# Kernel tuning notes

Hardware: AMD Instinct MI355X
Metric: run time of the kernel (lower is better)

Reference implementation:

```python
import jax, jax.numpy as jnp
import numpy as np

B, C, H, W = 4, 256, 64, 64
DQK = C // 8  # 32
EPS = 1e-5

def conv1x1(x, Wt, b):
    # 1x1 conv == per-pixel channel matmul. x: [B,C,H,W], Wt: [O,C], b: [O]
    return jnp.einsum('bchw,oc->bohw', x, Wt) + b[None, :, None, None]

def setup_inputs() -> dict:
    key = jax.random.key(0)
    ks = jax.random.split(key, 4)
    s = 1.0 / np.sqrt(C)
    return {
        'x': jax.random.normal(ks[0], (B, C, H, W), dtype=jnp.float32),
        'Wq': jax.random.normal(ks[1], (DQK, C), dtype=jnp.float32) * s,
        'bq': jnp.zeros((DQK,), dtype=jnp.float32),
        'Wk': jax.random.normal(ks[2], (DQK, C), dtype=jnp.float32) * s,
        'bk': jnp.zeros((DQK,), dtype=jnp.float32),
        'Wv': jax.random.normal(ks[3], (C, C), dtype=jnp.float32) * s,
        'bv': jnp.zeros((C,), dtype=jnp.float32),
        'bn_gamma': jnp.ones((C,), dtype=jnp.float32),
        'bn_beta': jnp.zeros((C,), dtype=jnp.float32),
    }

def reference(x, Wq, bq, Wk, bk, Wv, bv, bn_gamma, bn_beta):
    b, c, h, w = x.shape
    n = h * w
    q = conv1x1(x, Wq, bq).reshape(b, -1, n)   # [B, C/8, N]
    k = conv1x1(x, Wk, bk).reshape(b, -1, n)   # [B, C/8, N]
    v = conv1x1(x, Wv, bv).reshape(b, -1, n)   # [B, C,   N]
    # attention_weights = softmax(Q^T K) over last dim (no 1/sqrt(d) scaling)
    attn = jax.nn.softmax(jnp.einsum('bdi,bdj->bij', q, k), axis=-1)  # [B,N,N]
    out = jnp.einsum('bci,bij->bcj', v, attn).reshape(b, c, h, w)
    # BatchNorm2d (training mode: batch stats over B,H,W, biased var)
    mean = jnp.mean(out, axis=(0, 2, 3), keepdims=True)
    var = jnp.var(out, axis=(0, 2, 3), keepdims=True)
    out = (out - mean) * jax.lax.rsqrt(var + EPS)
    out = out * bn_gamma[None, :, None, None] + bn_beta[None, :, None, None]
    return x + out * 1e-05
```

## Files before the change

### kernel.cpp

```cpp
#include <hip/hip_runtime.h>
#include <hip/hip_bf16.h>

#define NB 4
#define NC 256
#define NN 4096

typedef __bf16 bf16x8 __attribute__((ext_vector_type(8)));
typedef float f32x4 __attribute__((ext_vector_type(4)));
typedef float f32x16 __attribute__((ext_vector_type(16)));
typedef unsigned short u16x4 __attribute__((ext_vector_type(4)));
typedef unsigned short u16x8 __attribute__((ext_vector_type(8)));
typedef unsigned int u32x2 __attribute__((ext_vector_type(2)));
typedef unsigned int u32x4 __attribute__((ext_vector_type(4)));

#if __has_builtin(__builtin_amdgcn_exp2f)
#define EXP2(x) __builtin_amdgcn_exp2f(x)
#else
#define EXP2(x) exp2f(x)
#endif

#define LOG2E 1.4426950408889634f

__device__ __forceinline__ unsigned short f2bf(float f) {
  union { __bf16 h; unsigned short u; } v;
  v.h = (__bf16)f;
  return v.u;
}
__device__ __forceinline__ float bf2f(unsigned short h) {
  union { unsigned u; float f; } v; v.u = ((unsigned)h) << 16;
  return v.f;
}

__device__ __forceinline__ u32x2 lane32swap(unsigned a, unsigned b) {
#if __has_builtin(__builtin_amdgcn_permlane32_swap)
  return __builtin_amdgcn_permlane32_swap(a, b, false, false);
#else
  unsigned ca = __shfl_xor(a, 32), cb = __shfl_xor(b, 32);
  int h = (threadIdx.x & 63) >> 5;
  u32x2 r; r[0] = h ? cb : a; r[1] = h ? b : ca;
  return r;
#endif
}

__global__ __launch_bounds__(256) void k0_prep(const float* __restrict__ Wq,
                                               const float* __restrict__ Wk,
                                               const float* __restrict__ Wv,
                                               unsigned short* __restrict__ Wcat,
                                               unsigned short* __restrict__ Wvb,
                                               float* __restrict__ stats) {
  int tid = blockIdx.x * 256 + threadIdx.x;
  int nt = gridDim.x * 256;
  for (int i = tid; i < 64 * NC; i += nt) {
    int d = i >> 8, c = i & 255;
    float v = (d < 32) ? Wq[d * NC + c] : Wk[(d - 32) * NC + c];
    Wcat[i] = f2bf(v);
  }
  for (int i = tid; i < NC * NC; i += nt) Wvb[i] = f2bf(Wv[i]);
  for (int i = tid; i < 1024; i += nt) stats[i] = 0.f;
}

__global__ __launch_bounds__(256) void k1_cvt_tr(const float* __restrict__ x,
                                                 unsigned short* __restrict__ xbf,
                                                 unsigned short* __restrict__ xT) {
  __shared__ __align__(16) unsigned short lt[64][68];
  int bid = blockIdx.x;
  int b  = bid >> 8;
  int cb = (bid >> 6) & 3;
  int nb = bid & 63;
  int c0 = cb * 64, n0 = nb * 64;
  int t = threadIdx.x;
  int tc = t >> 4;
  int tn = (t & 15) * 4;
#pragma unroll
  for (int it = 0; it < 4; ++it) {
    int c = c0 + tc + it * 16;
    f32x4 xv = *reinterpret_cast<const f32x4*>(&x[((size_t)b * NC + c) * NN + n0 + tn]);
    u16x4 hv;
    hv[0] = f2bf(xv[0]); hv[1] = f2bf(xv[1]); hv[2] = f2bf(xv[2]); hv[3] = f2bf(xv[3]);
    *reinterpret_cast<u16x4*>(&xbf[((size_t)b * NC + c) * NN + n0 + tn]) = hv;
    *reinterpret_cast<u16x4*>(&lt[tc + it * 16][tn]) = hv;
  }
  __syncthreads();
  int nl = t >> 2;
  int cl0 = (t & 3) * 16;
  u16x8 o0, o1;
#pragma unroll
  for (int q = 0; q < 8; ++q) o0[q] = lt[cl0 + q][nl];
#pragma unroll
  for (int q = 0; q < 8; ++q) o1[q] = lt[cl0 + 8 + q][nl];
  size_t ro = ((size_t)b * NN + n0 + nl) * NC + c0 + cl0;
  *reinterpret_cast<u16x8*>(&xT[ro]) = o0;
  *reinterpret_cast<u16x8*>(&xT[ro + 8]) = o1;
}

__global__ __launch_bounds__(256, 2) void k2_qk(const unsigned short* __restrict__ xT,
                                                const unsigned short* __restrict__ Wcat,
                                                const float* __restrict__ bq,
                                                const float* __restrict__ bk,
                                                unsigned short* __restrict__ Qt,
                                                unsigned short* __restrict__ Kt) {
  __shared__ __align__(16) unsigned short lt2[64][72];
  int bid = blockIdx.x;
  int b = bid >> 6, it = bid & 63;
  int i0 = it * 64;
  int t = threadIdx.x;
  int w = t >> 6, l = t & 63, l15 = l & 15, g = l >> 4;

  f32x4 acc[4];
#pragma unroll
  for (int f = 0; f < 4; ++f) acc[f] = f32x4{0.f, 0.f, 0.f, 0.f};

  const unsigned short* xrow = &xT[((size_t)b * NN + i0 + w * 16 + l15) * NC];
#pragma unroll
  for (int ks = 0; ks < 8; ++ks) {
    bf16x8 a = *reinterpret_cast<const bf16x8*>(&xrow[ks * 32 + g * 8]);
#pragma unroll
    for (int f = 0; f < 4; ++f) {
      bf16x8 bb = *reinterpret_cast<const bf16x8*>(&Wcat[(f * 16 + l15) * NC + ks * 32 + g * 8]);
      acc[f] = __builtin_amdgcn_mfma_f32_16x16x32_bf16(a, bb, acc[f], 0, 0, 0);
    }
  }
#pragma unroll
  for (int f = 0; f < 4; ++f) {
    int d = f * 16 + l15;
    float bias = (f < 2) ? bq[d] : bk[d - 32];
    float scale = (f < 2) ? LOG2E : 1.0f;
#pragma unroll
    for (int r = 0; r < 4; ++r)
      lt2[w * 16 + g * 4 + r][d] = f2bf((acc[f][r] + bias) * scale);
  }
  __syncthreads();
  int il = t >> 2, quad = t & 3;
  u32x4 v0 = *reinterpret_cast<const u32x4*>(&lt2[il][quad * 16]);
  u32x4 v1 = *reinterpret_cast<const u32x4*>(&lt2[il][quad * 16 + 8]);
  unsigned short* dst = (quad < 2) ? &Qt[((size_t)b * NN + i0 + il) * 32 + quad * 16]
                                   : &Kt[((size_t)b * NN + i0 + il) * 32 + (quad - 2) * 16];
  *reinterpret_cast<u32x4*>(dst) = v0;
  *reinterpret_cast<u32x4*>(&dst[8]) = v1;
}

__global__ __launch_bounds__(256, 4) void k3_rowsum(const unsigned short* __restrict__ Qt,
                                                    const unsigned short* __restrict__ Kt,
                                                    float* __restrict__ Lrow) {
  __shared__ float sred[4][16];
  int bid = blockIdx.x;
  int b = bid >> 8, it = bid & 255;
  int i0 = it * 16;
  int t = threadIdx.x, w = t >> 6, l = t & 63, l15 = l & 15, g = l >> 4;
  bf16x8 a = *reinterpret_cast<const bf16x8*>(&Qt[((size_t)b * NN + i0 + l15) * 32 + g * 8]);
  float rs0 = 0.f, rs1 = 0.f, rs2 = 0.f, rs3 = 0.f;
  int jbase = w * 1024;
  for (int jc = 0; jc < 16; ++jc) {
    int jb = jbase + jc * 64;
#pragma unroll
    for (int f = 0; f < 4; ++f) {
      bf16x8 bb = *reinterpret_cast<const bf16x8*>(&Kt[((size_t)b * NN + jb + f * 16 + l15) * 32 + g * 8]);
      f32x4 s = __builtin_amdgcn_mfma_f32_16x16x32_bf16(a, bb, f32x4{0.f, 0.f, 0.f, 0.f}, 0, 0, 0);
      rs0 += EXP2(s[0]); rs1 += EXP2(s[1]); rs2 += EXP2(s[2]); rs3 += EXP2(s[3]);
    }
  }
#pragma unroll
  for (int m = 1; m < 16; m <<= 1) {
    rs0 += __shfl_xor(rs0, m); rs1 += __shfl_xor(rs1, m);
    rs2 += __shfl_xor(rs2, m); rs3 += __shfl_xor(rs3, m);
  }
  if (l15 == 0) {
    sred[w][g * 4 + 0] = rs0; sred[w][g * 4 + 1] = rs1;
    sred[w][g * 4 + 2] = rs2; sred[w][g * 4 + 3] = rs3;
  }
  __syncthreads();
  if (t < 16) {
    float d = sred[0][t] + sred[1][t] + sred[2][t] + sred[3][t];
    Lrow[(size_t)b * NN + i0 + t] = -__log2f(d);
  }
}

__global__ __launch_bounds__(256, 2) void k4_attn(const unsigned short* __restrict__ xbf,
                                                  const unsigned short* __restrict__ Qt,
                                                  const unsigned short* __restrict__ Kt,
                                                  const float* __restrict__ Lrow,
                                                  unsigned short* __restrict__ Tt,
                                                  float* __restrict__ scol) {
  __shared__ __align__(16) unsigned short xlds[2][16384];
  int bid = blockIdx.x;
  int ih = bid & 1;
  int b  = (bid >> 1) & 3;
  int jt = bid >> 3;
  int t = threadIdx.x, w = t >> 6;
  int jw = w >> 1, cw = w & 1;
  int l = t & 63, l31 = l & 31, h = l >> 5;
  int j0 = jt * 64 + jw * 32;
  int c0 = cw * 128;
  const size_t qbase = (size_t)b * NN;
  unsigned short* Tt_p = Tt + (size_t)ih * ((size_t)NB * NN * NC);
  float* scol_p = scol + (size_t)ih * (NB * NN);
  int i0base = ih * 2048;
  int crow = t >> 3;
  int slot = t & 7;

  bf16x8 bk0 = *reinterpret_cast<const bf16x8*>(&Kt[(qbase + j0 + l31) * 32 + h * 8]);
  bf16x8 bk1 = *reinterpret_cast<const bf16x8*>(&Kt[(qbase + j0 + l31) * 32 + 16 + h * 8]);

  f32x16 acc0 = {0}, acc1 = {0}, acc2 = {0}, acc3 = {0};
  float cs = 0.f;
  u32x4 sreg0, sreg1, sreg2, sreg3, sreg4, sreg5, sreg6, sreg7;

#define REGLOAD(ibase_)                                                              \
  {                                                                                  \
    const unsigned short* xb_ = &xbf[(size_t)b * NC * NN + (ibase_) + slot * 8];     \
    sreg0 = *reinterpret_cast<const u32x4*>(&xb_[(size_t)(0 * 32 + crow) * NN]);     \
    sreg1 = *reinterpret_cast<const u32x4*>(&xb_[(size_t)(1 * 32 + crow) * NN]);     \
    sreg2 = *reinterpret_cast<const u32x4*>(&xb_[(size_t)(2 * 32 + crow) * NN]);     \
    sreg3 = *reinterpret_cast<const u32x4*>(&xb_[(size_t)(3 * 32 + crow) * NN]);     \
    sreg4 = *reinterpret_cast<const u32x4*>(&xb_[(size_t)(4 * 32 + crow) * NN]);     \
    sreg5 = *reinterpret_cast<const u32x4*>(&xb_[(size_t)(5 * 32 + crow) * NN]);     \
    sreg6 = *reinterpret_cast<const u32x4*>(&xb_[(size_t)(6 * 32 + crow) * NN]);     \
    sreg7 = *reinterpret_cast<const u32x4*>(&xb_[(size_t)(7 * 32 + crow) * NN]);     \
  }

#define DSWRITE(buf_)                                                                \
  {                                                                                  \
    int gsw_ = (slot ^ (crow & 7)) * 8;                                              \
    unsigned short* lb_ = &xlds[buf_][crow * 64 + gsw_];                             \
    *reinterpret_cast<u32x4*>(&lb_[0 * 2048]) = sreg0;                               \
    *reinterpret_cast<u32x4*>(&lb_[1 * 2048]) = sreg1;                               \
    *reinterpret_cast<u32x4*>(&lb_[2 * 2048]) = sreg2;                               \
    *reinterpret_cast<u32x4*>(&lb_[3 * 2048]) = sreg3;                               \
    *reinterpret_cast<u32x4*>(&lb_[4 * 2048]) = sreg4;                               \
    *reinterpret_cast<u32x4*>(&lb_[5 * 2048]) = sreg5;                               \
    *reinterpret_cast<u32x4*>(&lb_[6 * 2048]) = sreg6;                               \
    *reinterpret_cast<u32x4*>(&lb_[7 * 2048]) = sreg7;                               \
  }

  REGLOAD(i0base);
  DSWRITE(0);
  __syncthreads();
  int buf = 0;

  for (int st = 0; st < 32; ++st) {
    int ibase = i0base + st * 64;
    if (st + 1 < 32) REGLOAD(ibase + 64);
    const unsigned short* xt = xlds[buf];
#pragma unroll
    for (int ks = 0; ks < 2; ++ks) {
      int isub = ibase + ks * 32;
      const float* Lb = &Lrow[qbase + isub + 4 * h];
      f32x4 l0 = *reinterpret_cast<const f32x4*>(&Lb[0]);
      f32x4 l1 = *reinterpret_cast<const f32x4*>(&Lb[8]);
      f32x4 l2 = *reinterpret_cast<const f32x4*>(&Lb[16]);
      f32x4 l3 = *reinterpret_cast<const f32x4*>(&Lb[24]);
      f32x16 s;
#pragma unroll
      for (int r = 0; r < 4; ++r) { s[r] = l0[r]; s[4 + r] = l1[r]; s[8 + r] = l2[r]; s[12 + r] = l3[r]; }
      bf16x8 aq0 = *reinterpret_cast<const bf16x8*>(&Qt[(qbase + isub + l31) * 32 + h * 8]);
      bf16x8 aq1 = *reinterpret_cast<const bf16x8*>(&Qt[(qbase + isub + l31) * 32 + 16 + h * 8]);
      s = __builtin_amdgcn_mfma_f32_32x32x16_bf16(aq0, bk0, s, 0, 0, 0);
      s = __builtin_amdgcn_mfma_f32_32x32x16_bf16(aq1, bk1, s, 0, 0, 0);
      float p[16];
#pragma unroll
      for (int r = 0; r < 16; ++r) { p[r] = EXP2(s[r]); cs += p[r]; }
      unsigned q[8];
#pragma unroll
      for (int k = 0; k < 8; ++k)
        q[k] = (unsigned)f2bf(p[2 * k]) | ((unsigned)f2bf(p[2 * k + 1]) << 16);
      u32x2 s02 = lane32swap(q[0], q[2]);
      u32x2 s13 = lane32swap(q[1], q[3]);
      u32x2 s46 = lane32swap(q[4], q[6]);
      u32x2 s57 = lane32swap(q[5], q[7]);
      union { u32x4 u; bf16x8 v; } bm0, bm1;
      bm0.u = u32x4{s02[0], s13[0], s02[1], s13[1]};
      bm1.u = u32x4{s46[0], s57[0], s46[1], s57[1]};
      int swl = l31 & 7;
#pragma unroll
      for (int m = 0; m < 2; ++m) {
        bf16x8 bp = m ? bm1.v : bm0.v;
        int gif = ks * 4 + m * 2 + h;
        int gsw = (gif ^ swl) * 8;
        const unsigned short* lr = &xt[(c0 + l31) * 64 + gsw];
        bf16x8 ax0 = *reinterpret_cast<const bf16x8*>(&lr[0 * 2048]);
        bf16x8 ax1 = *reinterpret_cast<const bf16x8*>(&lr[1 * 2048]);
        bf16x8 ax2 = *reinterpret_cast<const bf16x8*>(&lr[2 * 2048]);
        bf16x8 ax3 = *reinterpret_cast<const bf16x8*>(&lr[3 * 2048]);
        acc0 = __builtin_amdgcn_mfma_f32_32x32x16_bf16(ax0, bp, acc0, 0, 0, 0);
        acc1 = __builtin_amdgcn_mfma_f32_32x32x16_bf16(ax1, bp, acc1, 0, 0, 0);
        acc2 = __builtin_amdgcn_mfma_f32_32x32x16_bf16(ax2, bp, acc2, 0, 0, 0);
        acc3 = __builtin_amdgcn_mfma_f32_32x32x16_bf16(ax3, bp, acc3, 0, 0, 0);
      }
    }
    if (st + 1 < 32) DSWRITE(buf ^ 1);
    __syncthreads();
    buf ^= 1;
  }
  cs += __shfl_xor(cs, 32);
  if (cw == 0 && l < 32) scol_p[qbase + j0 + l] = cs;
#pragma unroll
  for (int ci = 0; ci < 4; ++ci) {
    f32x16 a = (ci == 0) ? acc0 : (ci == 1) ? acc1 : (ci == 2) ? acc2 : acc3;
    unsigned qq[8];
#pragma unroll
    for (int k = 0; k < 8; ++k)
      qq[k] = (unsigned)f2bf(a[2 * k]) | ((unsigned)f2bf(a[2 * k + 1]) << 16);
    u32x2 t02 = lane32swap(qq[0], qq[2]);
    u32x2 t13 = lane32swap(qq[1], qq[3]);
    u32x2 t46 = lane32swap(qq[4], qq[6]);
    u32x2 t57 = lane32swap(qq[5], qq[7]);
    size_t row = (qbase + j0 + l31) * NC + c0 + ci * 32 + 8 * h;
    *reinterpret_cast<u32x4*>(&Tt_p[row])      = u32x4{t02[0], t13[0], t02[1], t13[1]};
    *reinterpret_cast<u32x4*>(&Tt_p[row + 16]) = u32x4{t46[0], t57[0], t46[1], t57[1]};
  }
#undef REGLOAD
#undef DSWRITE
}

__global__ __launch_bounds__(256, 2) void k5_out(const unsigned short* __restrict__ Wvb,
                                                 const unsigned short* __restrict__ Tt,
                                                 const float* __restrict__ scol,
                                                 const float* __restrict__ bv,
                                                 unsigned short* __restrict__ outbf) {
  int bid = blockIdx.x;
  int b = bid >> 7, jt = bid & 127;
  int j0 = jt * 32;
  int t = threadIdx.x, w = t >> 6, l = t & 63, l15 = l & 15, g = l >> 4;
  f32x4 acc[4][2];
#pragma unroll
  for (int ci = 0; ci < 4; ++ci)
#pragma unroll
    for (int f = 0; f < 2; ++f) acc[ci][f] = f32x4{0.f, 0.f, 0.f, 0.f};

#pragma unroll
  for (int ks = 0; ks < 8; ++ks) {
    bf16x8 a[4];
#pragma unroll
    for (int ci = 0; ci < 4; ++ci)
      a[ci] = *reinterpret_cast<const bf16x8*>(&Wvb[(w * 64 + ci * 16 + l15) * NC + ks * 32 + g * 8]);
#pragma unroll
    for (int h = 0; h < 2; ++h) {
      const unsigned short* T = Tt + (size_t)h * ((size_t)NB * NN * NC);
      bf16x8 bb[2];
#pragma unroll
      for (int f = 0; f < 2; ++f)
        bb[f] = *reinterpret_cast<const bf16x8*>(&T[((size_t)b * NN + j0 + f * 16 + l15) * NC + ks * 32 + g * 8]);
#pragma unroll
      for (int ci = 0; ci < 4; ++ci) {
        acc[ci][0] = __builtin_amdgcn_mfma_f32_16x16x32_bf16(a[ci], bb[0], acc[ci][0], 0, 0, 0);
        acc[ci][1] = __builtin_amdgcn_mfma_f32_16x16x32_bf16(a[ci], bb[1], acc[ci][1], 0, 0, 0);
      }
    }
  }
  float sv[2];
#pragma unroll
  for (int f = 0; f < 2; ++f) {
    size_t ji = (size_t)b * NN + j0 + f * 16 + l15;
    sv[f] = scol[ji] + scol[(size_t)NB * NN + ji];
  }
#pragma unroll
  for (int ci = 0; ci < 4; ++ci) {
    f32x4 bv4 = *reinterpret_cast<const f32x4*>(&bv[w * 64 + ci * 16 + g * 4]);
#pragma unroll
    for (int r = 0; r < 4; ++r) {
      int c = w * 64 + ci * 16 + g * 4 + r;
#pragma unroll
      for (int f = 0; f < 2; ++f)
        outbf[((size_t)b * NC + c) * NN + j0 + f * 16 + l15] = f2bf(acc[ci][f][r] + bv4[r] * sv[f]);
    }
  }
}

__global__ __launch_bounds__(256) void k5a_stats(const unsigned short* __restrict__ outbf,
                                                 float* __restrict__ stats) {
  __shared__ float sred[2][4];
  int c = blockIdx.x >> 1, half = blockIdx.x & 1;
  int t = threadIdx.x;
  float sum = 0.f, sq = 0.f;
#pragma unroll
  for (int b = 0; b < 4; ++b) {
    u16x8 v = *reinterpret_cast<const u16x8*>(
        &outbf[((((size_t)b << 8) + c) << 12) + half * 2048 + t * 8]);
#pragma unroll
    for (int q = 0; q < 8; ++q) {
      float f = bf2f(v[q]);
      sum += f; sq = fmaf(f, f, sq);
    }
  }
#pragma unroll
  for (int m = 1; m < 64; m <<= 1) {
    sum += __shfl_xor(sum, m); sq += __shfl_xor(sq, m);
  }
  if ((t & 63) == 0) { sred[0][t >> 6] = sum; sred[1][t >> 6] = sq; }
  __syncthreads();
  if (t == 0) {
    atomicAdd(&stats[c],       sred[0][0] + sred[0][1] + sred[0][2] + sred[0][3]);
    atomicAdd(&stats[256 + c], sred[1][0] + sred[1][1] + sred[1][2] + sred[1][3]);
  }
}

__global__ __launch_bounds__(256) void k6_fin(const float* __restrict__ gamma,
                                              const float* __restrict__ beta,
                                              float* __restrict__ stats) {
  int c = threadIdx.x;
  float mean = stats[c] * (1.0f / 16384.0f);
  float var = stats[256 + c] * (1.0f / 16384.0f) - mean * mean;
  float rstd = rsqrtf(var + 1e-5f);
  float sc = gamma[c] * rstd;
  stats[512 + c] = sc * 1e-5f;
  stats[768 + c] = (beta[c] - mean * sc) * 1e-5f;
}

__global__ __launch_bounds__(256) void k7_final(const float* __restrict__ x,
                                                const unsigned short* __restrict__ outbf,
                                                const float* __restrict__ stats,
                                                float* __restrict__ y) {
  int tid = blockIdx.x * 256 + threadIdx.x;
  size_t base = (size_t)tid * 8;
  int c = (int)((base >> 12) & 255);
  float sc = stats[512 + c], sh = stats[768 + c];
  u16x8 ov = *reinterpret_cast<const u16x8*>(&outbf[base]);
  f32x4 x0 = *reinterpret_cast<const f32x4*>(&x[base]);
  f32x4 x1 = *reinterpret_cast<const f32x4*>(&x[base + 4]);
  f32x4 y0, y1;
#pragma unroll
  for (int q = 0; q < 4; ++q) y0[q] = x0[q] + bf2f(ov[q]) * sc + sh;
#pragma unroll
  for (int q = 0; q < 4; ++q) y1[q] = x1[q] + bf2f(ov[4 + q]) * sc + sh;
  *reinterpret_cast<f32x4*>(&y[base]) = y0;
  *reinterpret_cast<f32x4*>(&y[base + 4]) = y1;
}

extern "C" void kernel_launch(void* const* d_in, const int* in_sizes, int n_in,
                              void* d_out, int out_size, void* d_ws, size_t ws_size,
                              hipStream_t stream) {
  (void)in_sizes; (void)n_in; (void)out_size;
  if (ws_size < 27627520) return;

  const float* x    = (const float*)d_in[0];
  const float* Wq   = (const float*)d_in[1];
  const float* bq   = (const float*)d_in[2];
  const float* Wk   = (const float*)d_in[3];
  const float* bk   = (const float*)d_in[4];
  const float* Wv   = (const float*)d_in[5];
  const float* bv   = (const float*)d_in[6];
  const float* gam  = (const float*)d_in[7];
  const float* bet  = (const float*)d_in[8];
  float* y = (float*)d_out;
  char* ws = (char*)d_ws;

  unsigned short* xbf  = (unsigned short*)(ws + 0);
  unsigned short* Tt   = (unsigned short*)(ws + 8388608);
  unsigned short* Qt   = (unsigned short*)(ws + 25165824);
  unsigned short* Kt   = (unsigned short*)(ws + 26214400);
  float* Lrow          = (float*)(ws + 27262976);
  float* scol          = (float*)(ws + 27328512);
  float* stats         = (float*)(ws + 27459584);
  unsigned short* Wcat = (unsigned short*)(ws + 27463680);
  unsigned short* Wvb  = (unsigned short*)(ws + 27496448);
  unsigned short* xT   = Tt;
  unsigned short* outbf = xbf;

  hipLaunchKernelGGL(k0_prep,  dim3(256),  dim3(256), 0, stream, Wq, Wk, Wv, Wcat, Wvb, stats);
  hipLaunchKernelGGL(k1_cvt_tr,dim3(1024), dim3(256), 0, stream, x, xbf, xT);
  hipLaunchKernelGGL(k2_qk,    dim3(256),  dim3(256), 0, stream, xT, Wcat, bq, bk, Qt, Kt);
  hipLaunchKernelGGL(k3_rowsum,dim3(1024), dim3(256), 0, stream, Qt, Kt, Lrow);
  hipLaunchKernelGGL(k4_attn,  dim3(512),  dim3(256), 0, stream, xbf, Qt, Kt, Lrow, Tt, scol);
  hipLaunchKernelGGL(k5_out,   dim3(512),  dim3(256), 0, stream, Wvb, Tt, scol, bv, outbf);
  hipLaunchKernelGGL(k5a_stats,dim3(512),  dim3(256), 0, stream, outbf, stats);
  hipLaunchKernelGGL(k6_fin,   dim3(1),    dim3(256), 0, stream, gam, bet, stats);
  hipLaunchKernelGGL(k7_final, dim3(2048), dim3(256), 0, stream, x, outbf, stats, y);
}
```

Measured before the change: 206.8 us.

## Fold weight prep and BN finalize into neighbours; widen attention blocks to 512 threads

Weight bf16 conversion moves into the transpose kernel, and the BN finalize step is folded into the final elementwise kernel. Per-channel stats are now written directly by one block per channel, with no atomics and no zeroing. Together these remove two launches. The attention kernel now runs 512-thread blocks covering 128 columns each at half the grid, so each staged x tile in LDS is shared by more warps. This risks lower occupancy and changes how loads are spread across threads.

```diff
diff --git a/kernel.cpp b/kernel.cpp
--- a/kernel.cpp
+++ b/kernel.cpp
@@ -42,27 +42,23 @@
 #endif
 }
 
-__global__ __launch_bounds__(256) void k0_prep(const float* __restrict__ Wq,
-                                               const float* __restrict__ Wk,
-                                               const float* __restrict__ Wv,
-                                               unsigned short* __restrict__ Wcat,
-                                               unsigned short* __restrict__ Wvb,
-                                               float* __restrict__ stats) {
-  int tid = blockIdx.x * 256 + threadIdx.x;
-  int nt = gridDim.x * 256;
-  for (int i = tid; i < 64 * NC; i += nt) {
-    int d = i >> 8, c = i & 255;
-    float v = (d < 32) ? Wq[d * NC + c] : Wk[(d - 32) * NC + c];
-    Wcat[i] = f2bf(v);
-  }
-  for (int i = tid; i < NC * NC; i += nt) Wvb[i] = f2bf(Wv[i]);
-  for (int i = tid; i < 1024; i += nt) stats[i] = 0.f;
-}
-
 __global__ __launch_bounds__(256) void k1_cvt_tr(const float* __restrict__ x,
+                                                 const float* __restrict__ Wq,
+                                                 const float* __restrict__ Wk,
+                                                 const float* __restrict__ Wv,
                                                  unsigned short* __restrict__ xbf,
-                                                 unsigned short* __restrict__ xT) {
+                                                 unsigned short* __restrict__ xT,
+                                                 unsigned short* __restrict__ Wcat,
+                                                 unsigned short* __restrict__ Wvb) {
   __shared__ __align__(16) unsigned short lt[64][68];
+  int gidx = blockIdx.x * 256 + threadIdx.x;
+  if (gidx < 64 * NC) {
+    int d = gidx >> 8, c = gidx & 255;
+    Wcat[gidx] = f2bf((d < 32) ? Wq[d * NC + c] : Wk[(d - 32) * NC + c]);
+  } else if (gidx < 64 * NC + NC * NC) {
+    int i = gidx - 64 * NC;
+    Wvb[i] = f2bf(Wv[i]);
+  }
   int bid = blockIdx.x;
   int b  = bid >> 8;
   int cb = (bid >> 6) & 3;
@@ -175,7 +171,7 @@
   }
 }
 
-__global__ __launch_bounds__(256, 2) void k4_attn(const unsigned short* __restrict__ xbf,
+__global__ __launch_bounds__(512, 2) void k4_attn(const unsigned short* __restrict__ xbf,
                                                   const unsigned short* __restrict__ Qt,
                                                   const unsigned short* __restrict__ Kt,
                                                   const float* __restrict__ Lrow,
@@ -189,7 +185,7 @@
   int t = threadIdx.x, w = t >> 6;
   int jw = w >> 1, cw = w & 1;
   int l = t & 63, l31 = l & 31, h = l >> 5;
-  int j0 = jt * 64 + jw * 32;
+  int j0 = jt * 128 + jw * 32;
   int c0 = cw * 128;
   const size_t qbase = (size_t)b * NN;
   unsigned short* Tt_p = Tt + (size_t)ih * ((size_t)NB * NN * NC);
@@ -203,33 +199,25 @@
 
   f32x16 acc0 = {0}, acc1 = {0}, acc2 = {0}, acc3 = {0};
   float cs = 0.f;
-  u32x4 sreg0, sreg1, sreg2, sreg3, sreg4, sreg5, sreg6, sreg7;
+  u32x4 sreg0, sreg1, sreg2, sreg3;
 
 #define REGLOAD(ibase_)                                                              \
   {                                                                                  \
     const unsigned short* xb_ = &xbf[(size_t)b * NC * NN + (ibase_) + slot * 8];     \
-    sreg0 = *reinterpret_cast<const u32x4*>(&xb_[(size_t)(0 * 32 + crow) * NN]);     \
-    sreg1 = *reinterpret_cast<const u32x4*>(&xb_[(size_t)(1 * 32 + crow) * NN]);     \
-    sreg2 = *reinterpret_cast<const u32x4*>(&xb_[(size_t)(2 * 32 + crow) * NN]);     \
-    sreg3 = *reinterpret_cast<const u32x4*>(&xb_[(size_t)(3 * 32 + crow) * NN]);     \
-    sreg4 = *reinterpret_cast<const u32x4*>(&xb_[(size_t)(4 * 32 + crow) * NN]);     \
-    sreg5 = *reinterpret_cast<const u32x4*>(&xb_[(size_t)(5 * 32 + crow) * NN]);     \
-    sreg6 = *reinterpret_cast<const u32x4*>(&xb_[(size_t)(6 * 32 + crow) * NN]);     \
-    sreg7 = *reinterpret_cast<const u32x4*>(&xb_[(size_t)(7 * 32 + crow) * NN]);     \
+    sreg0 = *reinterpret_cast<const u32x4*>(&xb_[(size_t)(0 * 64 + crow) * NN]);     \
+    sreg1 = *reinterpret_cast<const u32x4*>(&xb_[(size_t)(1 * 64 + crow) * NN]);     \
+    sreg2 = *reinterpret_cast<const u32x4*>(&xb_[(size_t)(2 * 64 + crow) * NN]);     \
+    sreg3 = *reinterpret_cast<const u32x4*>(&xb_[(size_t)(3 * 64 + crow) * NN]);     \
   }
 
 #define DSWRITE(buf_)                                                                \
   {                                                                                  \
     int gsw_ = (slot ^ (crow & 7)) * 8;                                              \
     unsigned short* lb_ = &xlds[buf_][crow * 64 + gsw_];                             \
-    *reinterpret_cast<u32x4*>(&lb_[0 * 2048]) = sreg0;                               \
-    *reinterpret_cast<u32x4*>(&lb_[1 * 2048]) = sreg1;                               \
-    *reinterpret_cast<u32x4*>(&lb_[2 * 2048]) = sreg2;                               \
-    *reinterpret_cast<u32x4*>(&lb_[3 * 2048]) = sreg3;                               \
-    *reinterpret_cast<u32x4*>(&lb_[4 * 2048]) = sreg4;                               \
-    *reinterpret_cast<u32x4*>(&lb_[5 * 2048]) = sreg5;                               \
-    *reinterpret_cast<u32x4*>(&lb_[6 * 2048]) = sreg6;                               \
-    *reinterpret_cast<u32x4*>(&lb_[7 * 2048]) = sreg7;                               \
+    *reinterpret_cast<u32x4*>(&lb_[0 * 4096]) = sreg0;                               \
+    *reinterpret_cast<u32x4*>(&lb_[1 * 4096]) = sreg1;                               \
+    *reinterpret_cast<u32x4*>(&lb_[2 * 4096]) = sreg2;                               \
+    *reinterpret_cast<u32x4*>(&lb_[3 * 4096]) = sreg3;                               \
   }
 
   REGLOAD(i0base);
@@ -369,17 +357,20 @@
 __global__ __launch_bounds__(256) void k5a_stats(const unsigned short* __restrict__ outbf,
                                                  float* __restrict__ stats) {
   __shared__ float sred[2][4];
-  int c = blockIdx.x >> 1, half = blockIdx.x & 1;
+  int c = blockIdx.x;
   int t = threadIdx.x;
   float sum = 0.f, sq = 0.f;
 #pragma unroll
   for (int b = 0; b < 4; ++b) {
-    u16x8 v = *reinterpret_cast<const u16x8*>(
-        &outbf[((((size_t)b << 8) + c) << 12) + half * 2048 + t * 8]);
-#pragma unroll
-    for (int q = 0; q < 8; ++q) {
-      float f = bf2f(v[q]);
-      sum += f; sq = fmaf(f, f, sq);
+#pragma unroll
+    for (int r = 0; r < 2; ++r) {
+      u16x8 v = *reinterpret_cast<const u16x8*>(
+          &outbf[((((size_t)b << 8) + c) << 12) + (size_t)(r * 256 + t) * 8]);
+#pragma unroll
+      for (int q = 0; q < 8; ++q) {
+        float f = bf2f(v[q]);
+        sum += f; sq = fmaf(f, f, sq);
+      }
     }
   }
 #pragma unroll
@@ -389,31 +380,26 @@
   if ((t & 63) == 0) { sred[0][t >> 6] = sum; sred[1][t >> 6] = sq; }
   __syncthreads();
   if (t == 0) {
-    atomicAdd(&stats[c],       sred[0][0] + sred[0][1] + sred[0][2] + sred[0][3]);
-    atomicAdd(&stats[256 + c], sred[1][0] + sred[1][1] + sred[1][2] + sred[1][3]);
-  }
-}
-
-__global__ __launch_bounds__(256) void k6_fin(const float* __restrict__ gamma,
-                                              const float* __restrict__ beta,
-                                              float* __restrict__ stats) {
-  int c = threadIdx.x;
-  float mean = stats[c] * (1.0f / 16384.0f);
-  float var = stats[256 + c] * (1.0f / 16384.0f) - mean * mean;
-  float rstd = rsqrtf(var + 1e-5f);
-  float sc = gamma[c] * rstd;
-  stats[512 + c] = sc * 1e-5f;
-  stats[768 + c] = (beta[c] - mean * sc) * 1e-5f;
+    stats[c]       = sred[0][0] + sred[0][1] + sred[0][2] + sred[0][3];
+    stats[256 + c] = sred[1][0] + sred[1][1] + sred[1][2] + sred[1][3];
+  }
 }
 
 __global__ __launch_bounds__(256) void k7_final(const float* __restrict__ x,
                                                 const unsigned short* __restrict__ outbf,
                                                 const float* __restrict__ stats,
+                                                const float* __restrict__ gamma,
+                                                const float* __restrict__ beta,
                                                 float* __restrict__ y) {
   int tid = blockIdx.x * 256 + threadIdx.x;
   size_t base = (size_t)tid * 8;
   int c = (int)((base >> 12) & 255);
-  float sc = stats[512 + c], sh = stats[768 + c];
+  float mean = stats[c] * (1.0f / 16384.0f);
+  float var = stats[256 + c] * (1.0f / 16384.0f) - mean * mean;
+  float rstd = rsqrtf(var + 1e-5f);
+  float g = gamma[c] * rstd;
+  float sc = g * 1e-5f;
+  float sh = (beta[c] - mean * g) * 1e-5f;
   u16x8 ov = *reinterpret_cast<const u16x8*>(&outbf[base]);
   f32x4 x0 = *reinterpret_cast<const f32x4*>(&x[base]);
   f32x4 x1 = *reinterpret_cast<const f32x4*>(&x[base + 4]);
@@ -456,13 +442,11 @@
   unsigned short* xT   = Tt;
   unsigned short* outbf = xbf;
 
-  hipLaunchKernelGGL(k0_prep,  dim3(256),  dim3(256), 0, stream, Wq, Wk, Wv, Wcat, Wvb, stats);
-  hipLaunchKernelGGL(k1_cvt_tr,dim3(1024), dim3(256), 0, stream, x, xbf, xT);
+  hipLaunchKernelGGL(k1_cvt_tr,dim3(1024), dim3(256), 0, stream, x, Wq, Wk, Wv, xbf, xT, Wcat, Wvb);
   hipLaunchKernelGGL(k2_qk,    dim3(256),  dim3(256), 0, stream, xT, Wcat, bq, bk, Qt, Kt);
   hipLaunchKernelGGL(k3_rowsum,dim3(1024), dim3(256), 0, stream, Qt, Kt, Lrow);
-  hipLaunchKernelGGL(k4_attn,  dim3(512),  dim3(256), 0, stream, xbf, Qt, Kt, Lrow, Tt, scol);
+  hipLaunchKernelGGL(k4_attn,  dim3(256),  dim3(512), 0, stream, xbf, Qt, Kt, Lrow, Tt, scol);
   hipLaunchKernelGGL(k5_out,   dim3(512),  dim3(256), 0, stream, Wvb, Tt, scol, bv, outbf);
-  hipLaunchKernelGGL(k5a_stats,dim3(512),  dim3(256), 0, stream, outbf, stats);
-  hipLaunchKernelGGL(k6_fin,   dim3(1),    dim3(256), 0, stream, gam, bet, stats);
-  hipLaunchKernelGGL(k7_final, dim3(2048), dim3(256), 0, stream, x, outbf, stats, y);
-}
+  hipLaunchKernelGGL(k5a_stats,dim3(256),  dim3(256), 0, stream, outbf, stats);
+  hipLaunchKernelGGL(k7_final, dim3(2048), dim3(256), 0, stream, x, outbf, stats, gam, bet, y);
+}
```

After: 216.9 us. 4.9% more time.
